# Performance work log

Hardware: AMD Instinct MI355X
Metric: run time of the kernel (lower is better)

The kernel has to match this reference:

```python
import jax, jax.numpy as jnp
import numpy as np

H, W_RFFT = 14, 8  # spatial grid 14x14, rfft2 last-dim width = 14//2+1


def setup_inputs() -> dict:
    key = jax.random.key(0)
    k1, k2 = jax.random.split(key)
    B, N, C = 256, 196, 512
    x = jax.random.normal(k1, (B, N, C), dtype=jnp.float32)
    complex_weight = jax.random.normal(k2, (H, W_RFFT, C, 2), dtype=jnp.float32) * 0.02
    return {"x": x, "complex_weight": complex_weight}


def reference(x, complex_weight):
    B, N, C = x.shape
    a = b = int(np.sqrt(N))  # 14
    xg = x.reshape(B, a, b, C).astype(jnp.float32)
    # rfft2 over spatial dims with ortho normalization
    xf = jnp.fft.rfft2(xg, axes=(1, 2), norm="ortho")  # [B, a, b//2+1, C] complex
    weight = complex_weight[..., 0] + 1j * complex_weight[..., 1]  # [a, b//2+1, C]
    xf = xf * weight
    xo = jnp.fft.irfft2(xf, s=(a, b), axes=(1, 2), norm="ortho")  # [B, a, b, C] real
    return xo.astype(x.dtype).reshape(B, N, C)
```

## Files before the change

kernel.cpp:

```cpp
#include <hip/hip_runtime.h>
#include <hip/hip_bf16.h>


#define Hs 14
#define Ns 196
#define Cc 512
#define CT 32
#define CONV_THREADS (CT * Hs)

__global__ __launch_bounds__(256) void prep_kernel(const float* __restrict__ cw,
                                                   float* __restrict__ R) {
    __shared__ float cs[14], sn[14];
    if (threadIdx.x < 14) {
        float ang = (float)threadIdx.x * 0.44879895051282760549f;
        cs[threadIdx.x] = cosf(ang);
        sn[threadIdx.x] = sinf(ang);
    }
    __syncthreads();

    int gid = blockIdx.x * 256 + threadIdx.x;
    int c = gid & 511;
    int s = gid >> 9;
    int dm = s / 14;
    int dn = s % 14;

    float acc = 0.0f;
    int kh = 0;
    for (int h = 0; h < 14; ++h) {
        int h2 = (h == 0) ? 0 : (14 - h);
        int k = kh;
        #pragma unroll
        for (int w = 0; w < 14; ++w) {
            float Ar, Ai;
            if (w <= 7) {
                const float* p = cw + (size_t)(((h * 8 + w) * 512 + c) * 2);
                Ar = p[0]; Ai = p[1];
            } else {
                const float* p = cw + (size_t)(((h2 * 8 + (14 - w)) * 512 + c) * 2);
                Ar = p[0]; Ai = -p[1];
            }
            acc += Ar * cs[k] - Ai * sn[k];
            k += dn; if (k >= 14) k -= 14;
        }
        kh += dm; if (kh >= 14) kh -= 14;
    }
    R[s * 512 + c] = acc * (1.0f / 196.0f);
}

__global__ __launch_bounds__(CONV_THREADS) void conv_kernel(
        const float* __restrict__ x,
        const float* __restrict__ R,
        float* __restrict__ out) {
    __shared__ float xs[Ns * CT];
    __shared__ float rs[Ns * CT];

    const int bx = blockIdx.x;
    const int ct = bx & 15;
    const int b  = bx >> 4;
    const int c0 = ct * CT;
    const int t  = threadIdx.x;

    const float* xb = x + (size_t)b * Ns * Cc + c0;
    const float* Rb = R + c0;
    for (int i = t; i < Ns * CT; i += CONV_THREADS) {
        int pq = i >> 5;
        int cc = i & (CT - 1);
        xs[pq * CT + cc] = xb[pq * Cc + cc];
        rs[pq * CT + cc] = Rb[pq * Cc + cc];
    }
    __syncthreads();

    const int c = t & (CT - 1);
    const int m = t >> 5;

    float acc[14];
    #pragma unroll
    for (int n = 0; n < 14; ++n) acc[n] = 0.0f;

    #pragma unroll 1
    for (int p = 0; p < 14; ++p) {
        int dm = m - p; if (dm < 0) dm += 14;
        float Rr[14];
        #pragma unroll
        for (int dn = 0; dn < 14; ++dn) Rr[dn] = rs[(dm * 14 + dn) * CT + c];
        #pragma unroll
        for (int q = 0; q < 14; ++q) {
            float xv = xs[(p * 14 + q) * CT + c];
            #pragma unroll
            for (int n = 0; n < 14; ++n) {
                acc[n] += xv * Rr[(n - q + 14) % 14];
            }
        }
    }

    float* ob = out + (size_t)b * Ns * Cc + (size_t)(m * 14) * Cc + c0 + c;
    #pragma unroll
    for (int n = 0; n < 14; ++n) ob[n * Cc] = acc[n];
}

extern "C" void kernel_launch(void* const* d_in, const int* in_sizes, int n_in,
                              void* d_out, int out_size, void* d_ws, size_t ws_size,
                              hipStream_t stream) {
    const float* x  = (const float*)d_in[0];
    const float* cw = (const float*)d_in[1];
    float* outp = (float*)d_out;
    float* R = (float*)d_ws;

    prep_kernel<<<392, 256, 0, stream>>>(cw, R);
    conv_kernel<<<256 * 16, CONV_THREADS, 0, stream>>>(x, R, outp);
}
```

Before: 296.1 us.

## Process two batches per block with packed v2f FMAs and separable filter prep

The conv kernel now handles two batch items per block. Each thread computes output rows m and m+7 using packed float2 accumulators, so the register-held filter rows are reused across two outputs and the compiler can emit packed FMA instructions. The filter prep is split into two separable 1D DFT passes through a workspace buffer, which removes the O(196) inner loop per element. In exchange there is an extra kernel launch and higher LDS and register use per block, with an occupancy hint of 3 blocks.

Measured after the change: 270.5 us. 8.7% less time.

```diff
diff --git a/kernel.cpp b/kernel.cpp
--- a/kernel.cpp
+++ b/kernel.cpp
@@ -6,10 +6,53 @@
 #define Ns 196
 #define Cc 512
 #define CT 32
-#define CONV_THREADS (CT * Hs)
+#define CONV_THREADS 448
 
-__global__ __launch_bounds__(256) void prep_kernel(const float* __restrict__ cw,
-                                                   float* __restrict__ R) {
+typedef float v2f __attribute__((ext_vector_type(2)));
+
+__global__ __launch_bounds__(256) void prep_a_kernel(const float* __restrict__ cw,
+                                                     float* __restrict__ T) {
+    __shared__ float cs[14], sn[14];
+    if (threadIdx.x < 14) {
+        float ang = (float)threadIdx.x * 0.44879895051282760549f;
+        cs[threadIdx.x] = cosf(ang);
+        sn[threadIdx.x] = sinf(ang);
+    }
+    __syncthreads();
+
+    int gid = blockIdx.x * 256 + threadIdx.x;
+    int c = gid & 511;
+    int s = gid >> 9;
+    int h = s / 14;
+    int dn = s % 14;
+    int h2 = (h == 0) ? 0 : (14 - h);
+
+    float Tr = 0.0f, Ti = 0.0f;
+    int k = 0;
+    #pragma unroll
+    for (int w = 0; w < 8; ++w) {
+        const float* p = cw + (size_t)(((h * 8 + w) * 512 + c) * 2);
+        float Wr = p[0], Wi = p[1];
+        Tr += Wr * cs[k] - Wi * sn[k];
+        Ti += Wr * sn[k] + Wi * cs[k];
+        k += dn; if (k >= 14) k -= 14;
+    }
+    int k2 = dn; if (k2 >= 14) k2 -= 14;
+    #pragma unroll
+    for (int w = 1; w < 7; ++w) {
+        const float* p = cw + (size_t)(((h2 * 8 + w) * 512 + c) * 2);
+        float Wr = p[0], Wi = p[1];
+        Tr += Wr * cs[k2] - Wi * sn[k2];
+        Ti -= Wr * sn[k2] + Wi * cs[k2];
+        k2 += dn; if (k2 >= 14) k2 -= 14;
+    }
+    float* o = T + (size_t)(s * 512 + c) * 2;
+    o[0] = Tr;
+    o[1] = Ti;
+}
+
+__global__ __launch_bounds__(256) void prep_b_kernel(const float* __restrict__ T,
+                                                     float* __restrict__ R) {
     __shared__ float cs[14], sn[14];
     if (threadIdx.x < 14) {
         float ang = (float)threadIdx.x * 0.44879895051282760549f;
@@ -26,76 +69,79 @@
 
     float acc = 0.0f;
     int kh = 0;
+    #pragma unroll
     for (int h = 0; h < 14; ++h) {
-        int h2 = (h == 0) ? 0 : (14 - h);
-        int k = kh;
-        #pragma unroll
-        for (int w = 0; w < 14; ++w) {
-            float Ar, Ai;
-            if (w <= 7) {
-                const float* p = cw + (size_t)(((h * 8 + w) * 512 + c) * 2);
-                Ar = p[0]; Ai = p[1];
-            } else {
-                const float* p = cw + (size_t)(((h2 * 8 + (14 - w)) * 512 + c) * 2);
-                Ar = p[0]; Ai = -p[1];
-            }
-            acc += Ar * cs[k] - Ai * sn[k];
-            k += dn; if (k >= 14) k -= 14;
-        }
+        const float* p = T + (size_t)(((h * 14 + dn) * 512 + c) * 2);
+        acc += p[0] * cs[kh] - p[1] * sn[kh];
         kh += dm; if (kh >= 14) kh -= 14;
     }
     R[s * 512 + c] = acc * (1.0f / 196.0f);
 }
 
-__global__ __launch_bounds__(CONV_THREADS) void conv_kernel(
+__global__ __launch_bounds__(CONV_THREADS, 3) void conv_kernel(
         const float* __restrict__ x,
         const float* __restrict__ R,
         float* __restrict__ out) {
-    __shared__ float xs[Ns * CT];
+    __shared__ float xs[2 * Ns * CT];
     __shared__ float rs[Ns * CT];
 
     const int bx = blockIdx.x;
     const int ct = bx & 15;
-    const int b  = bx >> 4;
+    const int bp = bx >> 4;
     const int c0 = ct * CT;
+    const int b0 = bp * 2;
     const int t  = threadIdx.x;
 
-    const float* xb = x + (size_t)b * Ns * Cc + c0;
+    const float* xb = x + (size_t)b0 * Ns * Cc + c0;
     const float* Rb = R + c0;
     for (int i = t; i < Ns * CT; i += CONV_THREADS) {
         int pq = i >> 5;
         int cc = i & (CT - 1);
-        xs[pq * CT + cc] = xb[pq * Cc + cc];
-        rs[pq * CT + cc] = Rb[pq * Cc + cc];
+        xs[i]           = xb[pq * Cc + cc];
+        xs[Ns * CT + i] = xb[Ns * Cc + pq * Cc + cc];
+        rs[i]           = Rb[pq * Cc + cc];
     }
     __syncthreads();
 
     const int c = t & (CT - 1);
-    const int m = t >> 5;
+    const int r = t >> 5;
+    const int bsel = (r >= 7) ? 1 : 0;
+    const int m = r - 7 * bsel;
+    const float* xsb = xs + bsel * Ns * CT;
 
-    float acc[14];
+    v2f acc[14];
     #pragma unroll
     for (int n = 0; n < 14; ++n) acc[n] = 0.0f;
 
     #pragma unroll 1
     for (int p = 0; p < 14; ++p) {
-        int dm = m - p; if (dm < 0) dm += 14;
-        float Rr[14];
+        int dm1 = m - p; if (dm1 < 0) dm1 += 14;
+        int dm2 = dm1 + 7; if (dm2 >= 14) dm2 -= 14;
+        v2f Rr[14];
         #pragma unroll
-        for (int dn = 0; dn < 14; ++dn) Rr[dn] = rs[(dm * 14 + dn) * CT + c];
+        for (int dn = 0; dn < 14; ++dn) {
+            Rr[dn].x = rs[(dm1 * 14 + dn) * CT + c];
+            Rr[dn].y = rs[(dm2 * 14 + dn) * CT + c];
+        }
         #pragma unroll
         for (int q = 0; q < 14; ++q) {
-            float xv = xs[(p * 14 + q) * CT + c];
+            float xv = xsb[(p * 14 + q) * CT + c];
+            v2f xv2 = {xv, xv};
             #pragma unroll
             for (int n = 0; n < 14; ++n) {
-                acc[n] += xv * Rr[(n - q + 14) % 14];
+                acc[n] += xv2 * Rr[(n - q + 14) % 14];
             }
         }
     }
 
-    float* ob = out + (size_t)b * Ns * Cc + (size_t)(m * 14) * Cc + c0 + c;
+    const int b = b0 + bsel;
+    float* o1 = out + ((size_t)b * Ns + m * 14) * Cc + c0 + c;
+    float* o2 = o1 + (size_t)(7 * 14) * Cc;
     #pragma unroll
-    for (int n = 0; n < 14; ++n) ob[n * Cc] = acc[n];
+    for (int n = 0; n < 14; ++n) {
+        o1[n * Cc] = acc[n].x;
+        o2[n * Cc] = acc[n].y;
+    }
 }
 
 extern "C" void kernel_launch(void* const* d_in, const int* in_sizes, int n_in,
@@ -105,7 +151,9 @@
     const float* cw = (const float*)d_in[1];
     float* outp = (float*)d_out;
     float* R = (float*)d_ws;
+    float* T = R + (size_t)Ns * Cc;
 
-    prep_kernel<<<392, 256, 0, stream>>>(cw, R);
-    conv_kernel<<<256 * 16, CONV_THREADS, 0, stream>>>(x, R, outp);
+    prep_a_kernel<<<392, 256, 0, stream>>>(cw, T);
+    prep_b_kernel<<<392, 256, 0, stream>>>(T, R);
+    conv_kernel<<<128 * 16, CONV_THREADS, 0, stream>>>(x, R, outp);
 }
```

## Share R tile across two batches, vectorize channel pairs, separable prep

Applied to the files above, without the earlier changes.

The conv kernel now processes two batch elements per block, so each R tile loaded into shared memory is reused twice. Each thread handles two adjacent channels with float2 loads and packed FMAs. The R tile is padded (stride 34) to change its shared-memory bank mapping, and launch bounds request three blocks per SM. The prep kernel computes the spatial kernel separably (row DFT into shared, then column DFT) instead of a direct double sum, cutting its arithmetic. The trade-off is more shared memory per block, which may limit occupancy, and halving the block count.

Measured after the change: 314.1 us. +6.1%, slower.

```diff
diff --git a/kernel.cpp b/kernel.cpp
--- a/kernel.cpp
+++ b/kernel.cpp
@@ -2,100 +2,132 @@
 #include <hip/hip_bf16.h>
 
 
-#define Hs 14
 #define Ns 196
 #define Cc 512
 #define CT 32
-#define CONV_THREADS (CT * Hs)
+#define RS_STRIDE 34
+#define CONV_THREADS 448
+
+typedef float v2f __attribute__((ext_vector_type(2)));
 
 __global__ __launch_bounds__(256) void prep_kernel(const float* __restrict__ cw,
                                                    float* __restrict__ R) {
+    __shared__ float Tr[Ns * 16], Ti[Ns * 16];
     __shared__ float cs[14], sn[14];
-    if (threadIdx.x < 14) {
-        float ang = (float)threadIdx.x * 0.44879895051282760549f;
-        cs[threadIdx.x] = cosf(ang);
-        sn[threadIdx.x] = sinf(ang);
+    const int t = threadIdx.x;
+    if (t < 14) {
+        float ang = (float)t * 0.44879895051282760549f;
+        cs[t] = cosf(ang);
+        sn[t] = sinf(ang);
     }
     __syncthreads();
 
-    int gid = blockIdx.x * 256 + threadIdx.x;
-    int c = gid & 511;
-    int s = gid >> 9;
-    int dm = s / 14;
-    int dn = s % 14;
+    const int c0 = blockIdx.x * 16;
 
-    float acc = 0.0f;
-    int kh = 0;
-    for (int h = 0; h < 14; ++h) {
+    for (int i = t; i < Ns * 16; i += 256) {
+        int cc = i & 15, s = i >> 4;
+        int h = s / 14, dn = s - h * 14;
         int h2 = (h == 0) ? 0 : (14 - h);
-        int k = kh;
+        float tr = 0.0f, ti = 0.0f;
+        int k = 0;
         #pragma unroll
-        for (int w = 0; w < 14; ++w) {
-            float Ar, Ai;
-            if (w <= 7) {
-                const float* p = cw + (size_t)(((h * 8 + w) * 512 + c) * 2);
-                Ar = p[0]; Ai = p[1];
-            } else {
-                const float* p = cw + (size_t)(((h2 * 8 + (14 - w)) * 512 + c) * 2);
-                Ar = p[0]; Ai = -p[1];
-            }
-            acc += Ar * cs[k] - Ai * sn[k];
+        for (int w = 0; w < 8; ++w) {
+            const float* p = cw + (size_t)(((h * 8 + w) * 512 + c0 + cc) * 2);
+            float Wr = p[0], Wi = p[1];
+            tr += Wr * cs[k] - Wi * sn[k];
+            ti += Wr * sn[k] + Wi * cs[k];
             k += dn; if (k >= 14) k -= 14;
         }
-        kh += dm; if (kh >= 14) kh -= 14;
+        int k2 = dn;
+        #pragma unroll
+        for (int w = 1; w < 7; ++w) {
+            const float* p = cw + (size_t)(((h2 * 8 + w) * 512 + c0 + cc) * 2);
+            float Wr = p[0], Wi = p[1];
+            tr += Wr * cs[k2] - Wi * sn[k2];
+            ti -= Wr * sn[k2] + Wi * cs[k2];
+            k2 += dn; if (k2 >= 14) k2 -= 14;
+        }
+        Tr[i] = tr; Ti[i] = ti;
     }
-    R[s * 512 + c] = acc * (1.0f / 196.0f);
+    __syncthreads();
+
+    for (int i = t; i < Ns * 16; i += 256) {
+        int cc = i & 15, s = i >> 4;
+        int dm = s / 14, dn = s - dm * 14;
+        float acc = 0.0f;
+        int kh = 0;
+        #pragma unroll
+        for (int h = 0; h < 14; ++h) {
+            int j = (h * 14 + dn) * 16 + cc;
+            acc += Tr[j] * cs[kh] - Ti[j] * sn[kh];
+            kh += dm; if (kh >= 14) kh -= 14;
+        }
+        R[s * 512 + c0 + cc] = acc * (1.0f / 196.0f);
+    }
 }
 
-__global__ __launch_bounds__(CONV_THREADS) void conv_kernel(
+__global__ __launch_bounds__(CONV_THREADS, 3) void conv_kernel(
         const float* __restrict__ x,
         const float* __restrict__ R,
         float* __restrict__ out) {
-    __shared__ float xs[Ns * CT];
-    __shared__ float rs[Ns * CT];
+    __shared__ float xs[2 * Ns * CT];
+    __shared__ float rs[Ns * RS_STRIDE];
 
     const int bx = blockIdx.x;
     const int ct = bx & 15;
-    const int b  = bx >> 4;
+    const int bp = bx >> 4;
     const int c0 = ct * CT;
+    const int b0 = bp * 2;
     const int t  = threadIdx.x;
 
-    const float* xb = x + (size_t)b * Ns * Cc + c0;
+    const float* xb = x + (size_t)b0 * Ns * Cc + c0;
     const float* Rb = R + c0;
     for (int i = t; i < Ns * CT; i += CONV_THREADS) {
-        int pq = i >> 5;
-        int cc = i & (CT - 1);
-        xs[pq * CT + cc] = xb[pq * Cc + cc];
-        rs[pq * CT + cc] = Rb[pq * Cc + cc];
+        int s = i >> 5, cc = i & 31;
+        xs[i]           = xb[s * Cc + cc];
+        xs[Ns * CT + i] = xb[(size_t)Ns * Cc + s * Cc + cc];
+        rs[s * RS_STRIDE + cc] = Rb[s * Cc + cc];
     }
     __syncthreads();
 
-    const int c = t & (CT - 1);
-    const int m = t >> 5;
+    const int cp   = t & 15;
+    const int r    = t >> 4;
+    const int m    = (r >= 14) ? (r - 14) : r;
+    const int bsel = (r >= 14) ? 1 : 0;
 
-    float acc[14];
+    const float* xsb = xs + bsel * Ns * CT + 2 * cp;
+    const float* rsc = rs + 2 * cp;
+
+    v2f acc[14];
     #pragma unroll
-    for (int n = 0; n < 14; ++n) acc[n] = 0.0f;
+    for (int n = 0; n < 14; ++n) acc[n] = (v2f)0.0f;
 
     #pragma unroll 1
     for (int p = 0; p < 14; ++p) {
         int dm = m - p; if (dm < 0) dm += 14;
-        float Rr[14];
+        const float* rrow = rsc + dm * (14 * RS_STRIDE);
+        v2f Rr[14];
         #pragma unroll
-        for (int dn = 0; dn < 14; ++dn) Rr[dn] = rs[(dm * 14 + dn) * CT + c];
+        for (int dn = 0; dn < 14; ++dn)
+            Rr[dn] = *(const v2f*)(rrow + dn * RS_STRIDE);
+
+        const float* xrow = xsb + p * (14 * CT);
         #pragma unroll
         for (int q = 0; q < 14; ++q) {
-            float xv = xs[(p * 14 + q) * CT + c];
+            v2f xv = *(const v2f*)(xrow + q * CT);
             #pragma unroll
             for (int n = 0; n < 14; ++n) {
-                acc[n] += xv * Rr[(n - q + 14) % 14];
+                int dn = n - q; if (dn < 0) dn += 14;
+                acc[n] = __builtin_elementwise_fma(xv, Rr[dn], acc[n]);
             }
         }
     }
 
-    float* ob = out + (size_t)b * Ns * Cc + (size_t)(m * 14) * Cc + c0 + c;
+    const int b = b0 + bsel;
+    float* ob = out + ((size_t)b * Ns + m * 14) * Cc + c0 + 2 * cp;
     #pragma unroll
-    for (int n = 0; n < 14; ++n) ob[n * Cc] = acc[n];
+    for (int n = 0; n < 14; ++n)
+        *(v2f*)(ob + n * Cc) = acc[n];
 }
 
 extern "C" void kernel_launch(void* const* d_in, const int* in_sizes, int n_in,
@@ -106,6 +138,6 @@
     float* outp = (float*)d_out;
     float* R = (float*)d_ws;
 
-    prep_kernel<<<392, 256, 0, stream>>>(cw, R);
-    conv_kernel<<<256 * 16, CONV_THREADS, 0, stream>>>(x, R, outp);
+    prep_kernel<<<32, 256, 0, stream>>>(cw, R);
+    conv_kernel<<<128 * 16, CONV_THREADS, 0, stream>>>(x, R, outp);
 }
```
